# Kernel tuning notes

Measured on AMD Instinct MI355X. Metric: run time of the kernel, lower is better.

Reference implementation:

```python
import jax, jax.numpy as jnp
from jax import lax
import numpy as np

DIM = 512; DEPTH = 2; DSTATE = 16; EXPAND = 4; NEXP = 4
DIN = DIM * EXPAND; DTRANK = (DIM + 15) // 16; DCONV = 4; HID = DIM * EXPAND
BATCH = 2; SEQ = 2048; CAP_FACTOR = 1.0; EPS = 1e-6


def setup_inputs():
    key = jax.random.key(0)
    ks = jax.random.split(key, 12)
    f = lambda k, s: jax.random.normal(k, s, jnp.float32) * 0.02
    return {
        "x": jax.random.normal(ks[0], (BATCH, SEQ, DIM), jnp.float32),
        "in_w": f(ks[1], (DEPTH, 2 * DIN, DIM)),
        "conv_w": f(ks[2], (DEPTH, DIN, 1, DCONV)),
        "conv_b": jnp.zeros((DEPTH, DIN), jnp.float32),
        "xproj_w": f(ks[3], (DEPTH, DTRANK + 2 * DSTATE, DIN)),
        "dt_w": f(ks[4], (DEPTH, DIN, DTRANK)),
        "dt_b": jnp.zeros((DEPTH, DIN), jnp.float32),
        "A_log": jnp.tile(jnp.log(jnp.arange(1, DSTATE + 1, dtype=jnp.float32))[None, None, :], (DEPTH, DIN, 1)),
        "Dp": jnp.ones((DEPTH, DIN), jnp.float32),
        "out_w": f(ks[5], (DEPTH, DIM, DIN)),
        "gate_w": f(ks[6], (DEPTH, NEXP, DIM)),
        "gate_b": jnp.zeros((DEPTH, NEXP), jnp.float32),
        "w1": f(ks[7], (DEPTH, NEXP, HID, DIM)),
        "b1": jnp.zeros((DEPTH, NEXP, HID), jnp.float32),
        "w2": f(ks[8], (DEPTH, NEXP, DIM, HID)),
        "b2": jnp.zeros((DEPTH, NEXP, DIM), jnp.float32),
    }


def _switch_moe(x, gw, gb, w1, b1, w2, b2):
    # zeta SwitchGate: softmax -> top-1 mask -> normalize by batch-dim sum, scale by capacity
    gs = jax.nn.softmax(jnp.einsum('bld,ed->ble', x, gw) + gb, axis=-1)  # (b,l,E)
    mask = jax.nn.one_hot(jnp.argmax(gs, axis=-1), NEXP, dtype=gs.dtype)
    masked = gs * mask
    capacity = int(CAP_FACTOR * x.shape[0])
    gate = masked / (masked.sum(axis=0, keepdims=True) + EPS) * capacity  # (b,l,E)
    # zeta SwitchMoE runs every expert on every token, then gate-weighted sum
    h = jax.nn.gelu(jnp.einsum('bld,ehd->bleh', x, w1) + b1, approximate=False)  # (b,l,E,HID)
    eo = jnp.einsum('bleh,edh->bled', h, w2) + b2                                 # (b,l,E,d)
    return jnp.einsum('bled,ble->bld', eo, gate)


def _mamba(x, in_w, conv_w, conv_b, xproj_w, dt_w, dt_b, A_log, Dp, out_w):
    b, l, d = x.shape
    xz = jnp.einsum('bld,ed->ble', x, in_w)   # (b,l,2*DIN)
    u, res = xz[..., :DIN], xz[..., DIN:]
    # causal depthwise conv: torch pads both sides by DCONV-1 then crops to L == left-pad only
    uc = lax.conv_general_dilated(u.transpose(0, 2, 1), conv_w, (1,), [(DCONV - 1, 0)],
                                  feature_group_count=DIN,
                                  dimension_numbers=('NCH', 'OIH', 'NCH'))
    u = jax.nn.silu((uc + conv_b[None, :, None]).transpose(0, 2, 1))  # (b,l,DIN)
    dbc = jnp.einsum('bld,ed->ble', u, xproj_w)                       # (b,l,DTRANK+2n)
    delta = jax.nn.softplus(jnp.einsum('blr,dr->bld', dbc[..., :DTRANK], dt_w) + dt_b)  # (b,l,DIN)
    B = dbc[..., DTRANK:DTRANK + DSTATE]
    C = dbc[..., DTRANK + DSTATE:]
    A = -jnp.exp(A_log)                                               # (DIN,n)

    def step(s, t):
        dt, Bt, Ct, ut = t  # (b,DIN),(b,n),(b,n),(b,DIN)
        s = jnp.exp(dt[:, :, None] * A) * s + (dt * ut)[:, :, None] * Bt[:, None, :]
        return s, jnp.einsum('bdn,bn->bd', s, Ct)

    s0 = jnp.zeros((b, DIN, DSTATE), x.dtype)
    _, ys = lax.scan(step, s0, (delta.transpose(1, 0, 2), B.transpose(1, 0, 2),
                                C.transpose(1, 0, 2), u.transpose(1, 0, 2)))
    y = ys.transpose(1, 0, 2) + u * Dp
    y = y * jax.nn.silu(res)
    return jnp.einsum('ble,de->bld', y, out_w)


def reference(x, in_w, conv_w, conv_b, xproj_w, dt_w, dt_b, A_log, Dp, out_w,
              gate_w, gate_b, w1, b1, w2, b2):
    for i in range(DEPTH):
        x = _switch_moe(x, gate_w[i], gate_b[i], w1[i], b1[i], w2[i], b2[i])
        x = _mamba(x, in_w[i], conv_w[i], conv_b[i], xproj_w[i], dt_w[i], dt_b[i],
                   A_log[i], Dp[i], out_w[i]) + x
        x = _switch_moe(x, gate_w[i], gate_b[i], w1[i], b1[i], w2[i], b2[i])
    return x
```

## Files before the change

kernel.cpp:

```cpp
#include <hip/hip_runtime.h>
#include <math.h>
#include <stdint.h>

typedef unsigned short u16;
typedef __attribute__((ext_vector_type(8))) _Float16 f16x8;
typedef __attribute__((ext_vector_type(4))) float f32x4;
typedef __attribute__((ext_vector_type(4))) u16 u16x4;

constexpr int DIM_    = 512;
constexpr int NEXP_   = 4;
constexpr int DIN_    = 2048;
constexpr int DTRANK_ = 32;
constexpr int DSTATE_ = 16;
constexpr int HID_    = 2048;
constexpr int BATCH_  = 2;
constexpr int SEQ_    = 2048;
constexpr int NTOK_   = BATCH_ * SEQ_;
constexpr float EPS_  = 1e-6f;

constexpr int NCHUNK_ = 32;
constexpr int CLEN_   = SEQ_ / NCHUNK_;

__device__ __forceinline__ float siluf(float x)     { return x / (1.f + __expf(-x)); }
__device__ __forceinline__ float geluf(float x)     { return 0.5f * x * (1.f + erff(x * 0.70710678118654752440f)); }
__device__ __forceinline__ float softplusf(float x) { return x > 20.f ? x : log1pf(__expf(x)); }

__device__ __forceinline__ float h2f(u16 b) { return (float)__builtin_bit_cast(_Float16, b); }
__device__ __forceinline__ void fsplit(float v, u16& h, u16& l) {
    _Float16 hh = (_Float16)v;
    float r = v - (float)hh;
    _Float16 ll = (_Float16)r;
    h = __builtin_bit_cast(u16, hh);
    l = __builtin_bit_cast(u16, ll);
}

__device__ __forceinline__ void gload16(const void* g, void* l) {
    __builtin_amdgcn_global_load_lds(
        (const __attribute__((address_space(1))) unsigned*)(uintptr_t)g,
        (__attribute__((address_space(3))) unsigned*)(uintptr_t)l,
        16, 0, 0);
}

enum { EPI_NONE = 0, EPI_GELU = 1, EPI_SCALE_BIAS = 2, EPI_RESID = 4 };

template <int TBM, int TBN, int EPI, bool OUTF32, bool SPLITK = false>
__global__ __launch_bounds__(256, 4) void gemm_split(
    const u16* __restrict__ Ah, const u16* __restrict__ Al, int lda,
    const u16* __restrict__ Wh, const u16* __restrict__ Wl, int ldw, long wstride,
    const float* __restrict__ bias, int bstride,
    u16* __restrict__ Ch, u16* __restrict__ Cl, float* __restrict__ Cf, int ldc,
    int M, int K,
    const int* __restrict__ counts, const int* __restrict__ perm, int permstride,
    const float* __restrict__ scale,
    const u16* __restrict__ Rh, const u16* __restrict__ Rl, int ldr)
{
    constexpr int BK  = 64;
    constexpr int CPR = 8;
    constexpr int RPI = 256 / CPR;
    constexpr int AISS = TBM / RPI;
    constexpr int BISS = TBN / RPI;
    constexpr int TM = TBM / 2;
    constexpr int TN = TBN / 2;
    constexpr int FM = TM / 16;
    constexpr int FN = TN / 16;

    const int e  = (SPLITK || !counts) ? 0 : blockIdx.z;
    const int Me = counts ? counts[e] : M;
    const int m0 = blockIdx.x * TBM;
    if (m0 >= Me) return;
    const int kbase = SPLITK ? blockIdx.z * K : 0;
    const int n0 = blockIdx.y * TBN;
    const int* rows = perm ? (perm + (long)e * permstride) : nullptr;
    const u16* Whe = Wh + (long)e * wstride;
    const u16* Wle = Wl + (long)e * wstride;
    const float* be = bias ? (bias + (long)e * bstride) : nullptr;
    float* Cfo = SPLITK ? (Cf + (size_t)blockIdx.z * M * ldc) : Cf;

    __shared__ __attribute__((aligned(16))) u16 AsH[TBM * BK], AsL[TBM * BK];
    __shared__ __attribute__((aligned(16))) u16 BsH[TBN * BK], BsL[TBN * BK];

    const int tid  = threadIdx.x;
    const int lane = tid & 63;
    const int wave = tid >> 6;
    const int wr = wave >> 1, wc = wave & 1;

    const int slot = tid & 7;
    const int rloc = tid >> 3;
    const int eoff = ((slot ^ (rloc & 7)) << 3) + kbase;
    const int ldst = tid * 8;

    long asrc[AISS];
#pragma unroll
    for (int i = 0; i < AISS; i++) {
        int gr = m0 + i * RPI + rloc;
        int src = rows ? rows[gr < Me ? gr : Me - 1] : gr;
        asrc[i] = (long)src * lda + eoff;
    }
    long bsrc[BISS];
#pragma unroll
    for (int i = 0; i < BISS; i++)
        bsrc[i] = (long)(n0 + i * RPI + rloc) * ldw + eoff;

    f32x4 zero = {0.f, 0.f, 0.f, 0.f};
    f32x4 acc[FM][FN];
#pragma unroll
    for (int m = 0; m < FM; m++)
#pragma unroll
        for (int n = 0; n < FN; n++) acc[m][n] = zero;

    const int lr = lane & 15;
    const int kq = (lane >> 4) * 8;

    for (int k0 = 0; k0 < K; k0 += BK) {
#pragma unroll
        for (int i = 0; i < AISS; i++) {
            gload16(Ah + asrc[i] + k0, &AsH[i * RPI * BK + ldst]);
            gload16(Al + asrc[i] + k0, &AsL[i * RPI * BK + ldst]);
        }
#pragma unroll
        for (int i = 0; i < BISS; i++) {
            gload16(Whe + bsrc[i] + k0, &BsH[i * RPI * BK + ldst]);
            gload16(Wle + bsrc[i] + k0, &BsL[i * RPI * BK + ldst]);
        }
        __syncthreads();
#pragma unroll
        for (int kk = 0; kk < 2; kk++) {
            const int lk = kk * 32 + kq;
            f16x8 ah[FM], al[FM], bh[FN], bl[FN];
#pragma unroll
            for (int m = 0; m < FM; m++) {
                int row = wr * TM + m * 16 + lr;
                int off = row * BK + (lk ^ ((row & 7) << 3));
                ah[m] = *(const f16x8*)&AsH[off];
                al[m] = *(const f16x8*)&AsL[off];
            }
#pragma unroll
            for (int n = 0; n < FN; n++) {
                int row = wc * TN + n * 16 + lr;
                int off = row * BK + (lk ^ ((row & 7) << 3));
                bh[n] = *(const f16x8*)&BsH[off];
                bl[n] = *(const f16x8*)&BsL[off];
            }
#pragma unroll
            for (int m = 0; m < FM; m++)
#pragma unroll
                for (int n = 0; n < FN; n++) {
                    acc[m][n] = __builtin_amdgcn_mfma_f32_16x16x32_f16(ah[m], bh[n], acc[m][n], 0, 0, 0);
                    acc[m][n] = __builtin_amdgcn_mfma_f32_16x16x32_f16(ah[m], bl[n], acc[m][n], 0, 0, 0);
                    acc[m][n] = __builtin_amdgcn_mfma_f32_16x16x32_f16(al[m], bh[n], acc[m][n], 0, 0, 0);
                }
        }
        __syncthreads();
    }

    const int rq = lane >> 4;
#pragma unroll
    for (int m = 0; m < FM; m++) {
#pragma unroll
        for (int n = 0; n < FN; n++) {
            const int col = n0 + wc * TN + n * 16 + lr;
            const float bv = be ? be[col] : 0.f;
#pragma unroll
            for (int r = 0; r < 4; r++) {
                const int gr = m0 + wr * TM + m * 16 + rq * 4 + r;
                if (gr >= Me) continue;
                const long crow = rows ? rows[gr] : gr;
                float v = acc[m][n][r];
                if constexpr (EPI == EPI_GELU)            v = geluf(v + bv);
                else if constexpr (EPI == EPI_SCALE_BIAS) v = scale[crow] * (v + bv);
                else if constexpr (EPI == EPI_RESID)
                    v += h2f(Rh[crow * ldr + col]) + h2f(Rl[crow * ldr + col]);
                if constexpr (OUTF32) {
                    Cfo[crow * ldc + col] = v;
                } else {
                    u16 hh, ll; fsplit(v, hh, ll);
                    Ch[crow * ldc + col] = hh;
                    Cl[crow * ldc + col] = ll;
                }
            }
        }
    }
}

__global__ __launch_bounds__(256) void sum4_kernel(
    const float* __restrict__ p, float* __restrict__ out, int n)
{
    int i = (blockIdx.x * 256 + threadIdx.x) * 4;
    if (i >= n) return;
    float4 a = *(const float4*)(p + i);
    float4 b = *(const float4*)(p + n + i);
    float4 c = *(const float4*)(p + 2 * (size_t)n + i);
    float4 d = *(const float4*)(p + 3 * (size_t)n + i);
    float4 o = make_float4(a.x + b.x + c.x + d.x, a.y + b.y + c.y + d.y,
                           a.z + b.z + c.z + d.z, a.w + b.w + c.w + d.w);
    *(float4*)(out + i) = o;
}

__global__ __launch_bounds__(256) void cvt_split(
    const float* __restrict__ in, u16* __restrict__ oh, u16* __restrict__ ol, int n)
{
    int i = (blockIdx.x * 256 + threadIdx.x) * 4;
    if (i >= n) return;
    float4 v = *(const float4*)(in + i);
    u16 h0, l0, h1, l1, h2, l2, h3, l3;
    fsplit(v.x, h0, l0); fsplit(v.y, h1, l1);
    fsplit(v.z, h2, l2); fsplit(v.w, h3, l3);
    u16x4 hv = {h0, h1, h2, h3}, lv = {l0, l1, l2, l3};
    *(u16x4*)(oh + i) = hv;
    *(u16x4*)(ol + i) = lv;
}

__global__ __launch_bounds__(128) void gate_kernel(
    const u16* __restrict__ Xh, const u16* __restrict__ Xl,
    const float* __restrict__ gw, const float* __restrict__ gb,
    float* __restrict__ gval, int* __restrict__ perm, int* __restrict__ counts)
{
    const int l    = blockIdx.x;
    const int wv   = threadIdx.x >> 6;
    const int lane = threadIdx.x & 63;
    const int t    = wv * SEQ_ + l;
    const size_t xb = (size_t)t * DIM_;
    float a0 = 0, a1 = 0, a2 = 0, a3 = 0;
    for (int k = lane; k < DIM_; k += 64) {
        float xv = h2f(Xh[xb + k]) + h2f(Xl[xb + k]);
        a0 += xv * gw[0 * DIM_ + k];
        a1 += xv * gw[1 * DIM_ + k];
        a2 += xv * gw[2 * DIM_ + k];
        a3 += xv * gw[3 * DIM_ + k];
    }
#pragma unroll
    for (int off = 32; off; off >>= 1) {
        a0 += __shfl_xor(a0, off);
        a1 += __shfl_xor(a1, off);
        a2 += __shfl_xor(a2, off);
        a3 += __shfl_xor(a3, off);
    }
    __shared__ float sval[2];
    __shared__ int   sidx[2];
    if (lane == 0) {
        float lg[4] = { a0 + gb[0], a1 + gb[1], a2 + gb[2], a3 + gb[3] };
        int bi = 0; float m = lg[0];
#pragma unroll
        for (int q = 1; q < 4; q++) if (lg[q] > m) { m = lg[q]; bi = q; }
        float s = 0.f;
#pragma unroll
        for (int q = 0; q < 4; q++) s += __expf(lg[q] - m);
        sval[wv] = 1.f / s;
        sidx[wv] = bi;
    }
    __syncthreads();
    if (lane == 0) {
        float myv = sval[wv]; int myi = sidx[wv];
        float ov  = sval[wv ^ 1]; int oi = sidx[wv ^ 1];
        float denom = myv + (oi == myi ? ov : 0.f) + EPS_;
        gval[t] = myv / denom * 2.0f;
        int pos = atomicAdd(&counts[myi], 1);
        perm[myi * NTOK_ + pos] = t;
    }
}

__global__ __launch_bounds__(256) void conv_silu_kernel(
    const float* __restrict__ xz, const float* __restrict__ cw,
    const float* __restrict__ cb, u16* __restrict__ Uh, u16* __restrict__ Ul)
{
    const long idx = (long)blockIdx.x * blockDim.x + threadIdx.x;
    const int c = (int)(idx & (DIN_ - 1));
    const int t = (int)(idx >> 11);
    const int l = t & (SEQ_ - 1);
    const float* base = xz + (size_t)t * (2 * DIN_) + c;
    float w0 = cw[c * 4 + 0], w1 = cw[c * 4 + 1], w2 = cw[c * 4 + 2], w3 = cw[c * 4 + 3];
    float acc = cb[c] + w3 * base[0];
    if (l >= 1) acc += w2 * base[-1L * (2 * DIN_)];
    if (l >= 2) acc += w1 * base[-2L * (2 * DIN_)];
    if (l >= 3) acc += w0 * base[-3L * (2 * DIN_)];
    float u = siluf(acc);
    u16 h, lo; fsplit(u, h, lo);
    Uh[idx] = h; Ul[idx] = lo;
}

__global__ __launch_bounds__(256) void gemm_dt(
    const float* __restrict__ A,
    const float* __restrict__ W,
    const float* __restrict__ bias,
    float* __restrict__ C)
{
    const int m0 = blockIdx.x * 64;
    const int n0 = blockIdx.y * 64;
    __shared__ float As[16][65];
    __shared__ float Bs[16][65];
    const int tid  = threadIdx.x;
    const int lrow = tid >> 2;
    const int lk4  = (tid & 3) << 2;
    const int tx   = tid & 15, ty = tid >> 4;
    const float* Aptr = A + (long)(m0 + lrow) * 64 + lk4;
    const float* Wptr = W + (long)(n0 + lrow) * 32 + lk4;
    float acc[4][4] = {};
    for (int k0 = 0; k0 < 32; k0 += 16) {
        float4 av = *(const float4*)(Aptr + k0);
        float4 wv = *(const float4*)(Wptr + k0);
        As[lk4 + 0][lrow] = av.x; As[lk4 + 1][lrow] = av.y;
        As[lk4 + 2][lrow] = av.z; As[lk4 + 3][lrow] = av.w;
        Bs[lk4 + 0][lrow] = wv.x; Bs[lk4 + 1][lrow] = wv.y;
        Bs[lk4 + 2][lrow] = wv.z; Bs[lk4 + 3][lrow] = wv.w;
        __syncthreads();
#pragma unroll
        for (int k = 0; k < 16; k++) {
            float a0 = As[k][ty * 4 + 0], a1 = As[k][ty * 4 + 1],
                  a2 = As[k][ty * 4 + 2], a3 = As[k][ty * 4 + 3];
            float b0 = Bs[k][tx * 4 + 0], b1 = Bs[k][tx * 4 + 1],
                  b2 = Bs[k][tx * 4 + 2], b3 = Bs[k][tx * 4 + 3];
            acc[0][0] += a0 * b0; acc[0][1] += a0 * b1; acc[0][2] += a0 * b2; acc[0][3] += a0 * b3;
            acc[1][0] += a1 * b0; acc[1][1] += a1 * b1; acc[1][2] += a1 * b2; acc[1][3] += a1 * b3;
            acc[2][0] += a2 * b0; acc[2][1] += a2 * b1; acc[2][2] += a2 * b2; acc[2][3] += a2 * b3;
            acc[3][0] += a3 * b0; acc[3][1] += a3 * b1; acc[3][2] += a3 * b2; acc[3][3] += a3 * b3;
        }
        __syncthreads();
    }
#pragma unroll
    for (int i = 0; i < 4; i++) {
        float4 out;
#pragma unroll
        for (int j = 0; j < 4; j++)
            (&out.x)[j] = softplusf(acc[i][j] + bias[n0 + tx * 4 + j]);
        *(float4*)(C + (long)(m0 + ty * 4 + i) * DIN_ + n0 + tx * 4) = out;
    }
}

__global__ __launch_bounds__(256) void scan_part(
    const float* __restrict__ delta,
    const u16* __restrict__ Uh, const u16* __restrict__ Ul,
    const float* __restrict__ dbc, const float* __restrict__ A_log,
    float* __restrict__ sloc, float* __restrict__ sdt)
{
    const int d = blockIdx.x * 256 + threadIdx.x;
    const int c = blockIdx.y;
    const int b = blockIdx.z;
    float Ad[DSTATE_];
#pragma unroll
    for (int n = 0; n < DSTATE_; n++) Ad[n] = -__expf(A_log[d * DSTATE_ + n]);
    float s[DSTATE_];
#pragma unroll
    for (int n = 0; n < DSTATE_; n++) s[n] = 0.f;
    float sumdt = 0.f;
    const int tbase = b * SEQ_ + c * CLEN_;
    for (int l = 0; l < CLEN_; l++) {
        const size_t idx = (size_t)(tbase + l) * DIN_ + d;
        const float dt = delta[idx];
        const float uu = h2f(Uh[idx]) + h2f(Ul[idx]);
        const float du = dt * uu;
        sumdt += dt;
        const float* bc = dbc + (size_t)(tbase + l) * 64;
#pragma unroll
        for (int n = 0; n < DSTATE_; n++)
            s[n] = __expf(dt * Ad[n]) * s[n] + du * bc[32 + n];
    }
    const int bc_ = b * NCHUNK_ + c;
#pragma unroll
    for (int n = 0; n < DSTATE_; n++)
        sloc[((size_t)bc_ * DSTATE_ + n) * DIN_ + d] = s[n];
    sdt[(size_t)bc_ * DIN_ + d] = sumdt;
}

__global__ __launch_bounds__(256) void scan_combine(
    float* __restrict__ sloc, const float* __restrict__ sdt,
    const float* __restrict__ A_log)
{
    const int id = blockIdx.x * 256 + threadIdx.x;
    const int d  = id & (DIN_ - 1);
    const int rest = id >> 11;
    const int n  = rest & (DSTATE_ - 1);
    const int b  = rest >> 4;
    const float Ad = -__expf(A_log[d * DSTATE_ + n]);
    float sin = 0.f;
    for (int c = 0; c < NCHUNK_; c++) {
        const int bc_ = b * NCHUNK_ + c;
        const size_t idx = ((size_t)bc_ * DSTATE_ + n) * DIN_ + d;
        const float slocal = sloc[idx];
        const float P = __expf(sdt[(size_t)bc_ * DIN_ + d] * Ad);
        sloc[idx] = sin;
        sin = P * sin + slocal;
    }
}

__global__ __launch_bounds__(256) void scan_final(
    const float* __restrict__ delta,
    u16* Uh, u16* Ul,
    const float* __restrict__ dbc, const float* __restrict__ A_log,
    const float* __restrict__ Dp, const float* __restrict__ xz,
    const float* __restrict__ sloc)
{
    const int d = blockIdx.x * 256 + threadIdx.x;
    const int c = blockIdx.y;
    const int b = blockIdx.z;
    float Ad[DSTATE_];
#pragma unroll
    for (int n = 0; n < DSTATE_; n++) Ad[n] = -__expf(A_log[d * DSTATE_ + n]);
    const float Dd = Dp[d];
    const int bc_ = b * NCHUNK_ + c;
    float s[DSTATE_];
#pragma unroll
    for (int n = 0; n < DSTATE_; n++)
        s[n] = sloc[((size_t)bc_ * DSTATE_ + n) * DIN_ + d];
    const int tbase = b * SEQ_ + c * CLEN_;
    for (int l = 0; l < CLEN_; l++) {
        const int t = tbase + l;
        const size_t idx = (size_t)t * DIN_ + d;
        const float dt = delta[idx];
        const float uu = h2f(Uh[idx]) + h2f(Ul[idx]);
        const float du = dt * uu;
        const float* bc = dbc + (size_t)t * 64;
        float sum = 0.f;
#pragma unroll
        for (int n = 0; n < DSTATE_; n++) {
            float sn = __expf(dt * Ad[n]) * s[n] + du * bc[32 + n];
            s[n] = sn;
            sum += sn * bc[48 + n];
        }
        const float res = xz[(size_t)t * (2 * DIN_) + DIN_ + d];
        float y = (sum + uu * Dd) * siluf(res);
        u16 hh, ll; fsplit(y, hh, ll);
        Uh[idx] = hh; Ul[idx] = ll;
    }
}

extern "C" void kernel_launch(void* const* d_in, const int* in_sizes, int n_in,
                              void* d_out, int out_size, void* d_ws, size_t ws_size,
                              hipStream_t stream)
{
    const float* x0      = (const float*)d_in[0];
    const float* in_w    = (const float*)d_in[1];
    const float* conv_w  = (const float*)d_in[2];
    const float* conv_b  = (const float*)d_in[3];
    const float* xproj_w = (const float*)d_in[4];
    const float* dt_w    = (const float*)d_in[5];
    const float* dt_b    = (const float*)d_in[6];
    const float* A_log   = (const float*)d_in[7];
    const float* Dp      = (const float*)d_in[8];
    const float* out_w   = (const float*)d_in[9];
    const float* gate_w  = (const float*)d_in[10];
    const float* gate_b  = (const float*)d_in[11];
    const float* w1      = (const float*)d_in[12];
    const float* b1      = (const float*)d_in[13];
    const float* w2      = (const float*)d_in[14];
    const float* b2      = (const float*)d_in[15];

    char* p = (char*)d_ws;
    auto carve = [&](size_t bytes) -> void* {
        void* r = (void*)p;
        p += (bytes + 255) & ~(size_t)255;
        return r;
    };
    const size_t NX = (size_t)NTOK_ * DIM_;
    const size_t NU = (size_t)NTOK_ * DIN_;
    u16* XaH = (u16*)carve(NX * 2); u16* XaL = (u16*)carve(NX * 2);
    u16* XbH = (u16*)carve(NX * 2); u16* XbL = (u16*)carve(NX * 2);
    float* xz    = (float*)carve((size_t)NTOK_ * 2 * DIN_ * 4);
    u16* UH  = (u16*)carve(NU * 2);
    u16* UL  = (u16*)carve(NU * 2);
    float* delta = (float*)carve(NU * 4);
    float* dbc   = (float*)carve((size_t)NTOK_ * 64 * 4);
    float* xpp   = (float*)carve((size_t)4 * NTOK_ * 64 * 4);
    float* sloc  = (float*)carve((size_t)BATCH_ * NCHUNK_ * DSTATE_ * DIN_ * 4);
    float* sdt   = (float*)carve((size_t)BATCH_ * NCHUNK_ * DIN_ * 4);
    float* gval  = (float*)carve((size_t)NTOK_ * 4);
    int*   perm  = (int*)carve((size_t)NEXP_ * NTOK_ * 4);
    int*   counts = (int*)carve(256);
    const size_t NW1 = (size_t)NEXP_ * HID_ * DIM_;
    u16* w1H = (u16*)carve(NW1 * 2); u16* w1L = (u16*)carve(NW1 * 2);
    u16* w2H = (u16*)carve(NW1 * 2); u16* w2L = (u16*)carve(NW1 * 2);
    const size_t NIW = (size_t)2 * DIN_ * DIM_;
    u16* iwH = (u16*)carve(NIW * 2); u16* iwL = (u16*)carve(NIW * 2);
    const size_t NOW = (size_t)DIM_ * DIN_;
    u16* owH = (u16*)carve(NOW * 2); u16* owL = (u16*)carve(NOW * 2);
    const size_t NXP = (size_t)64 * DIN_;
    u16* xpH = (u16*)carve(NXP * 2); u16* xpL = (u16*)carve(NXP * 2);

    auto cvt = [&](const float* in, u16* oh, u16* ol, size_t n) {
        cvt_split<<<(unsigned)((n / 4 + 255) / 256), 256, 0, stream>>>(in, oh, ol, (int)n);
    };

    auto moe = [&](const u16* Xh, const u16* Xl, u16* Oh, u16* Ol, float* Of, int dep) {
        hipMemsetAsync(counts, 0, NEXP_ * sizeof(int), stream);
        gate_kernel<<<SEQ_, 128, 0, stream>>>(
            Xh, Xl, gate_w + (size_t)dep * NEXP_ * DIM_, gate_b + dep * NEXP_,
            gval, perm, counts);
        gemm_split<64, 128, EPI_GELU, false><<<dim3(NTOK_ / 64, HID_ / 128, NEXP_), 256, 0, stream>>>(
            Xh, Xl, DIM_, w1H, w1L, DIM_, (long)HID_ * DIM_,
            b1 + (size_t)dep * NEXP_ * HID_, HID_,
            UH, UL, nullptr, HID_, NTOK_, DIM_,
            counts, perm, NTOK_, nullptr, nullptr, nullptr, 0);
        if (Of) {
            gemm_split<64, 64, EPI_SCALE_BIAS, true><<<dim3(NTOK_ / 64, DIM_ / 64, NEXP_), 256, 0, stream>>>(
                UH, UL, HID_, w2H, w2L, HID_, (long)DIM_ * HID_,
                b2 + (size_t)dep * NEXP_ * DIM_, DIM_,
                nullptr, nullptr, Of, DIM_, NTOK_, HID_,
                counts, perm, NTOK_, gval, nullptr, nullptr, 0);
        } else {
            gemm_split<64, 64, EPI_SCALE_BIAS, false><<<dim3(NTOK_ / 64, DIM_ / 64, NEXP_), 256, 0, stream>>>(
                UH, UL, HID_, w2H, w2L, HID_, (long)DIM_ * HID_,
                b2 + (size_t)dep * NEXP_ * DIM_, DIM_,
                Oh, Ol, nullptr, DIM_, NTOK_, HID_,
                counts, perm, NTOK_, gval, nullptr, nullptr, 0);
        }
    };

    auto mamba = [&](const u16* Xh, const u16* Xl, u16* Oh, u16* Ol, int dep) {
        gemm_split<64, 128, EPI_NONE, true><<<dim3(NTOK_ / 64, (2 * DIN_) / 128, 1), 256, 0, stream>>>(
            Xh, Xl, DIM_, iwH, iwL, DIM_, 0, nullptr, 0,
            nullptr, nullptr, xz, 2 * DIN_, NTOK_, DIM_,
            nullptr, nullptr, 0, nullptr, nullptr, nullptr, 0);
        conv_silu_kernel<<<(NTOK_ * DIN_) / 256, 256, 0, stream>>>(
            xz, conv_w + (size_t)dep * DIN_ * 4, conv_b + dep * DIN_, UH, UL);
        gemm_split<64, 64, EPI_NONE, true, true><<<dim3(NTOK_ / 64, 1, 4), 256, 0, stream>>>(
            UH, UL, DIN_, xpH, xpL, DIN_, 0, nullptr, 0,
            nullptr, nullptr, xpp, 64, NTOK_, DIN_ / 4,
            nullptr, nullptr, 0, nullptr, nullptr, nullptr, 0);
        sum4_kernel<<<(NTOK_ * 64) / 1024, 256, 0, stream>>>(xpp, dbc, NTOK_ * 64);
        gemm_dt<<<dim3(NTOK_ / 64, DIN_ / 64), 256, 0, stream>>>(
            dbc, dt_w + (size_t)dep * DIN_ * DTRANK_, dt_b + dep * DIN_, delta);
        const float* Al = A_log + (size_t)dep * DIN_ * DSTATE_;
        scan_part<<<dim3(DIN_ / 256, NCHUNK_, BATCH_), 256, 0, stream>>>(
            delta, UH, UL, dbc, Al, sloc, sdt);
        scan_combine<<<(BATCH_ * DSTATE_ * DIN_) / 256, 256, 0, stream>>>(sloc, sdt, Al);
        scan_final<<<dim3(DIN_ / 256, NCHUNK_, BATCH_), 256, 0, stream>>>(
            delta, UH, UL, dbc, Al, Dp + dep * DIN_, xz, sloc);
        gemm_split<64, 64, EPI_RESID, false><<<dim3(NTOK_ / 64, DIM_ / 64, 1), 256, 0, stream>>>(
            UH, UL, DIN_, owH, owL, DIN_, 0, nullptr, 0,
            Oh, Ol, nullptr, DIM_, NTOK_, DIN_,
            nullptr, nullptr, 0, nullptr, Xh, Xl, DIM_);
    };

    cvt(x0, XaH, XaL, NX);
    for (int dep = 0; dep < 2; dep++) {
        cvt(in_w + (size_t)dep * NIW, iwH, iwL, NIW);
        cvt(xproj_w + (size_t)dep * NXP, xpH, xpL, NXP);
        cvt(out_w + (size_t)dep * NOW, owH, owL, NOW);
        cvt(w1 + (size_t)dep * NW1, w1H, w1L, NW1);
        cvt(w2 + (size_t)dep * NW1, w2H, w2L, NW1);
        if (dep == 0) {
            moe(XaH, XaL, XbH, XbL, nullptr, 0);
            mamba(XbH, XbL, XaH, XaL, 0);
            moe(XaH, XaL, XbH, XbL, nullptr, 0);
        } else {
            moe(XbH, XbL, XaH, XaL, nullptr, 1);
            mamba(XaH, XaL, XbH, XbL, 1);
            moe(XbH, XbL, nullptr, nullptr, (float*)d_out, 1);
        }
    }
}
```

Measured before the change: 1.481 ms.

## Double-buffer GEMM LDS tiles, fix 64x64 tiles, and remap blocks across XCDs

The split-precision GEMM now fixes every tile at 64x64 and double-buffers the A/B shared-memory tiles, so the global-to-LDS load of the next K step overlaps the MFMA work on the current one. Workgroup IDs are remapped so consecutive logical tiles land on the same XCD, which is meant to improve L2 reuse. Launch bounds drop to 2 blocks per CU because LDS use doubles. The 128-wide launches become 64-wide with twice as many blocks, which adds operand reloads. The loop also still has only one barrier per iteration, so the next prefetch can overwrite a buffer other waves may still be reading, a possible race.

Result: slower. 1.527 ms (+3.1%).

```diff
diff --git a/kernel.cpp b/kernel.cpp
--- a/kernel.cpp
+++ b/kernel.cpp
@@ -43,8 +43,8 @@
 
 enum { EPI_NONE = 0, EPI_GELU = 1, EPI_SCALE_BIAS = 2, EPI_RESID = 4 };
 
-template <int TBM, int TBN, int EPI, bool OUTF32, bool SPLITK = false>
-__global__ __launch_bounds__(256, 4) void gemm_split(
+template <int EPI, bool OUTF32, bool SPLITK = false>
+__global__ __launch_bounds__(256, 2) void gemm_split(
     const u16* __restrict__ Ah, const u16* __restrict__ Al, int lda,
     const u16* __restrict__ Wh, const u16* __restrict__ Wl, int ldw, long wstride,
     const float* __restrict__ bias, int bstride,
@@ -54,30 +54,32 @@
     const float* __restrict__ scale,
     const u16* __restrict__ Rh, const u16* __restrict__ Rl, int ldr)
 {
-    constexpr int BK  = 64;
-    constexpr int CPR = 8;
-    constexpr int RPI = 256 / CPR;
-    constexpr int AISS = TBM / RPI;
-    constexpr int BISS = TBN / RPI;
-    constexpr int TM = TBM / 2;
-    constexpr int TN = TBN / 2;
-    constexpr int FM = TM / 16;
-    constexpr int FN = TN / 16;
-
-    const int e  = (SPLITK || !counts) ? 0 : blockIdx.z;
+    const int nwg = gridDim.x * gridDim.y * gridDim.z;
+    int lid = blockIdx.x + gridDim.x * (blockIdx.y + gridDim.y * blockIdx.z);
+    {
+        const int q = nwg >> 3, r = nwg & 7;
+        const int xcd = lid & 7, idx = lid >> 3;
+        lid = (xcd < r ? xcd * (q + 1) : r * (q + 1) + (xcd - r) * q) + idx;
+    }
+    const int bx = lid % gridDim.x;
+    const int rest = lid / gridDim.x;
+    const int by = rest % gridDim.y;
+    const int bz = rest / gridDim.y;
+
+    const int e  = (SPLITK || !counts) ? 0 : bz;
     const int Me = counts ? counts[e] : M;
-    const int m0 = blockIdx.x * TBM;
+    const int m0 = bx * 64;
     if (m0 >= Me) return;
-    const int kbase = SPLITK ? blockIdx.z * K : 0;
-    const int n0 = blockIdx.y * TBN;
+    const int kbase = SPLITK ? bz * K : 0;
+    const int n0 = by * 64;
     const int* rows = perm ? (perm + (long)e * permstride) : nullptr;
     const u16* Whe = Wh + (long)e * wstride;
     const u16* Wle = Wl + (long)e * wstride;
     const float* be = bias ? (bias + (long)e * bstride) : nullptr;
-    float* Cfo = SPLITK ? (Cf + (size_t)blockIdx.z * M * ldc) : Cf;
-
-    __shared__ __attribute__((aligned(16))) u16 AsH[TBM * BK], AsL[TBM * BK];
-    __shared__ __attribute__((aligned(16))) u16 BsH[TBN * BK], BsL[TBN * BK];
+    float* Cfo = SPLITK ? (Cf + (size_t)bz * M * ldc) : Cf;
+
+    __shared__ __attribute__((aligned(16))) u16 AsH[2][4096], AsL[2][4096];
+    __shared__ __attribute__((aligned(16))) u16 BsH[2][4096], BsL[2][4096];
 
     const int tid  = threadIdx.x;
     const int lane = tid & 63;
@@ -89,62 +91,67 @@
     const int eoff = ((slot ^ (rloc & 7)) << 3) + kbase;
     const int ldst = tid * 8;
 
-    long asrc[AISS];
-#pragma unroll
-    for (int i = 0; i < AISS; i++) {
-        int gr = m0 + i * RPI + rloc;
+    long asrc[2];
+#pragma unroll
+    for (int i = 0; i < 2; i++) {
+        int gr = m0 + i * 32 + rloc;
         int src = rows ? rows[gr < Me ? gr : Me - 1] : gr;
         asrc[i] = (long)src * lda + eoff;
     }
-    long bsrc[BISS];
-#pragma unroll
-    for (int i = 0; i < BISS; i++)
-        bsrc[i] = (long)(n0 + i * RPI + rloc) * ldw + eoff;
+    long bsrc[2];
+#pragma unroll
+    for (int i = 0; i < 2; i++)
+        bsrc[i] = (long)(n0 + i * 32 + rloc) * ldw + eoff;
+
+    auto stage = [&](int buf, int k0) {
+#pragma unroll
+        for (int i = 0; i < 2; i++) {
+            gload16(Ah + asrc[i] + k0, &AsH[buf][i * 2048 + ldst]);
+            gload16(Al + asrc[i] + k0, &AsL[buf][i * 2048 + ldst]);
+            gload16(Whe + bsrc[i] + k0, &BsH[buf][i * 2048 + ldst]);
+            gload16(Wle + bsrc[i] + k0, &BsL[buf][i * 2048 + ldst]);
+        }
+    };
 
     f32x4 zero = {0.f, 0.f, 0.f, 0.f};
-    f32x4 acc[FM][FN];
-#pragma unroll
-    for (int m = 0; m < FM; m++)
-#pragma unroll
-        for (int n = 0; n < FN; n++) acc[m][n] = zero;
+    f32x4 acc[2][2];
+#pragma unroll
+    for (int m = 0; m < 2; m++)
+#pragma unroll
+        for (int n = 0; n < 2; n++) acc[m][n] = zero;
 
     const int lr = lane & 15;
     const int kq = (lane >> 4) * 8;
 
-    for (int k0 = 0; k0 < K; k0 += BK) {
-#pragma unroll
-        for (int i = 0; i < AISS; i++) {
-            gload16(Ah + asrc[i] + k0, &AsH[i * RPI * BK + ldst]);
-            gload16(Al + asrc[i] + k0, &AsL[i * RPI * BK + ldst]);
-        }
-#pragma unroll
-        for (int i = 0; i < BISS; i++) {
-            gload16(Whe + bsrc[i] + k0, &BsH[i * RPI * BK + ldst]);
-            gload16(Wle + bsrc[i] + k0, &BsL[i * RPI * BK + ldst]);
-        }
-        __syncthreads();
+    const int NT = K / 64;
+    stage(0, 0);
+    __syncthreads();
+
+    for (int t = 0; t < NT; ++t) {
+        const int buf = t & 1;
+        if (t + 1 < NT) stage(buf ^ 1, (t + 1) * 64);
 #pragma unroll
         for (int kk = 0; kk < 2; kk++) {
             const int lk = kk * 32 + kq;
-            f16x8 ah[FM], al[FM], bh[FN], bl[FN];
-#pragma unroll
-            for (int m = 0; m < FM; m++) {
-                int row = wr * TM + m * 16 + lr;
-                int off = row * BK + (lk ^ ((row & 7) << 3));
-                ah[m] = *(const f16x8*)&AsH[off];
-                al[m] = *(const f16x8*)&AsL[off];
+            f16x8 ah[2], al[2], bh[2], bl[2];
+#pragma unroll
+            for (int m = 0; m < 2; m++) {
+                int row = wr * 32 + m * 16 + lr;
+                int off = row * 64 + (lk ^ ((row & 7) << 3));
+                ah[m] = *(const f16x8*)&AsH[buf][off];
+                al[m] = *(const f16x8*)&AsL[buf][off];
             }
 #pragma unroll
-            for (int n = 0; n < FN; n++) {
-                int row = wc * TN + n * 16 + lr;
-                int off = row * BK + (lk ^ ((row & 7) << 3));
-                bh[n] = *(const f16x8*)&BsH[off];
-                bl[n] = *(const f16x8*)&BsL[off];
+            for (int n = 0; n < 2; n++) {
+                int row = wc * 32 + n * 16 + lr;
+                int off = row * 64 + (lk ^ ((row & 7) << 3));
+                bh[n] = *(const f16x8*)&BsH[buf][off];
+                bl[n] = *(const f16x8*)&BsL[buf][off];
             }
 #pragma unroll
-            for (int m = 0; m < FM; m++)
-#pragma unroll
-                for (int n = 0; n < FN; n++) {
+            for (int m = 0; m < 2; m++)
+#pragma unroll
+                for (int n = 0; n < 2; n++) {
                     acc[m][n] = __builtin_amdgcn_mfma_f32_16x16x32_f16(ah[m], bh[n], acc[m][n], 0, 0, 0);
                     acc[m][n] = __builtin_amdgcn_mfma_f32_16x16x32_f16(ah[m], bl[n], acc[m][n], 0, 0, 0);
                     acc[m][n] = __builtin_amdgcn_mfma_f32_16x16x32_f16(al[m], bh[n], acc[m][n], 0, 0, 0);
@@ -155,14 +162,14 @@
 
     const int rq = lane >> 4;
 #pragma unroll
-    for (int m = 0; m < FM; m++) {
-#pragma unroll
-        for (int n = 0; n < FN; n++) {
-            const int col = n0 + wc * TN + n * 16 + lr;
+    for (int m = 0; m < 2; m++) {
+#pragma unroll
+        for (int n = 0; n < 2; n++) {
+            const int col = n0 + wc * 32 + n * 16 + lr;
             const float bv = be ? be[col] : 0.f;
 #pragma unroll
             for (int r = 0; r < 4; r++) {
-                const int gr = m0 + wr * TM + m * 16 + rq * 4 + r;
+                const int gr = m0 + wr * 32 + m * 16 + rq * 4 + r;
                 if (gr >= Me) continue;
                 const long crow = rows ? rows[gr] : gr;
                 float v = acc[m][n][r];
@@ -484,19 +491,19 @@
         gate_kernel<<<SEQ_, 128, 0, stream>>>(
             Xh, Xl, gate_w + (size_t)dep * NEXP_ * DIM_, gate_b + dep * NEXP_,
             gval, perm, counts);
-        gemm_split<64, 128, EPI_GELU, false><<<dim3(NTOK_ / 64, HID_ / 128, NEXP_), 256, 0, stream>>>(
+        gemm_split<EPI_GELU, false><<<dim3(NTOK_ / 64, HID_ / 64, NEXP_), 256, 0, stream>>>(
             Xh, Xl, DIM_, w1H, w1L, DIM_, (long)HID_ * DIM_,
             b1 + (size_t)dep * NEXP_ * HID_, HID_,
             UH, UL, nullptr, HID_, NTOK_, DIM_,
             counts, perm, NTOK_, nullptr, nullptr, nullptr, 0);
         if (Of) {
-            gemm_split<64, 64, EPI_SCALE_BIAS, true><<<dim3(NTOK_ / 64, DIM_ / 64, NEXP_), 256, 0, stream>>>(
+            gemm_split<EPI_SCALE_BIAS, true><<<dim3(NTOK_ / 64, DIM_ / 64, NEXP_), 256, 0, stream>>>(
                 UH, UL, HID_, w2H, w2L, HID_, (long)DIM_ * HID_,
                 b2 + (size_t)dep * NEXP_ * DIM_, DIM_,
                 nullptr, nullptr, Of, DIM_, NTOK_, HID_,
                 counts, perm, NTOK_, gval, nullptr, nullptr, 0);
         } else {
-            gemm_split<64, 64, EPI_SCALE_BIAS, false><<<dim3(NTOK_ / 64, DIM_ / 64, NEXP_), 256, 0, stream>>>(
+            gemm_split<EPI_SCALE_BIAS, false><<<dim3(NTOK_ / 64, DIM_ / 64, NEXP_), 256, 0, stream>>>(
                 UH, UL, HID_, w2H, w2L, HID_, (long)DIM_ * HID_,
                 b2 + (size_t)dep * NEXP_ * DIM_, DIM_,
                 Oh, Ol, nullptr, DIM_, NTOK_, HID_,
@@ -505,13 +512,13 @@
     };
 
     auto mamba = [&](const u16* Xh, const u16* Xl, u16* Oh, u16* Ol, int dep) {
-        gemm_split<64, 128, EPI_NONE, true><<<dim3(NTOK_ / 64, (2 * DIN_) / 128, 1), 256, 0, stream>>>(
+        gemm_split<EPI_NONE, true><<<dim3(NTOK_ / 64, (2 * DIN_) / 64, 1), 256, 0, stream>>>(
             Xh, Xl, DIM_, iwH, iwL, DIM_, 0, nullptr, 0,
             nullptr, nullptr, xz, 2 * DIN_, NTOK_, DIM_,
             nullptr, nullptr, 0, nullptr, nullptr, nullptr, 0);
         conv_silu_kernel<<<(NTOK_ * DIN_) / 256, 256, 0, stream>>>(
             xz, conv_w + (size_t)dep * DIN_ * 4, conv_b + dep * DIN_, UH, UL);
-        gemm_split<64, 64, EPI_NONE, true, true><<<dim3(NTOK_ / 64, 1, 4), 256, 0, stream>>>(
+        gemm_split<EPI_NONE, true, true><<<dim3(NTOK_ / 64, 1, 4), 256, 0, stream>>>(
             UH, UL, DIN_, xpH, xpL, DIN_, 0, nullptr, 0,
             nullptr, nullptr, xpp, 64, NTOK_, DIN_ / 4,
             nullptr, nullptr, 0, nullptr, nullptr, nullptr, 0);
@@ -524,7 +531,7 @@
         scan_combine<<<(BATCH_ * DSTATE_ * DIN_) / 256, 256, 0, stream>>>(sloc, sdt, Al);
         scan_final<<<dim3(DIN_ / 256, NCHUNK_, BATCH_), 256, 0, stream>>>(
             delta, UH, UL, dbc, Al, Dp + dep * DIN_, xz, sloc);
-        gemm_split<64, 64, EPI_RESID, false><<<dim3(NTOK_ / 64, DIM_ / 64, 1), 256, 0, stream>>>(
+        gemm_split<EPI_RESID, false><<<dim3(NTOK_ / 64, DIM_ / 64, 1), 256, 0, stream>>>(
             UH, UL, DIN_, owH, owL, DIN_, 0, nullptr, 0,
             Oh, Ol, nullptr, DIM_, NTOK_, DIN_,
             nullptr, nullptr, 0, nullptr, Xh, Xl, DIM_);
```
